# Performance work log

Measured on AMD Instinct MI355X. Metric: run time of the kernel, lower is better.

Reference implementation:

```python
import jax, jax.numpy as jnp
import numpy as np

B = 128
K = 16
# (in_ch, featdim, dim) per stage, matching conv1..conv11
DIMS = [(3, 8, 2048), (8, 32, 1024), (32, 64, 512), (64, 64, 256), (64, 64, 128),
        (64, 128, 64), (128, 256, 32), (256, 512, 16), (512, 512, 8), (512, 512, 4),
        (512, 1024, 2)]


def setup_inputs() -> dict:
    key = jax.random.key(0)
    ks = jax.random.split(key, 64)
    inp = {"x": jax.random.normal(ks[0], (B, 3, 2048), dtype=jnp.float32)}
    i = 1
    for li, (cin, cf, d) in enumerate(DIMS, start=1):
        inp[f"W{li}"] = jax.random.normal(ks[i], (3 * cf, cin), dtype=jnp.float32) / np.sqrt(cin).astype(np.float32); i += 1
        inp[f"b{li}"] = jax.random.normal(ks[i], (3 * cf,), dtype=jnp.float32) * 0.01; i += 1
        inp[f"sel{li}"] = jax.random.randint(ks[i], (d,), 0, 3); i += 1
    inp["fcW"] = jax.random.normal(ks[i], (K, 1024), dtype=jnp.float32) / np.sqrt(1024).astype(np.float32); i += 1
    inp["fcb"] = jax.random.normal(ks[i], (K,), dtype=jnp.float32) * 0.01
    return inp


def kdconv(x, W, b, sel, featdim, dim):
    # 1x1 conv == per-position matmul: x [B, Cin, dim] -> y [B, 3*featdim, dim]
    y = jax.nn.relu(jnp.einsum('oi,bin->bon', W, x) + b[None, :, None])
    y = y.reshape(-1, featdim, 3, dim)
    # kd split-dim gather: pick one of the 3 feature groups per position
    y = jnp.take_along_axis(y, sel[None, None, None, :], axis=2)[:, :, 0, :]  # [B, featdim, dim]
    # pairwise max-pool of sibling leaves
    return y.reshape(-1, featdim, dim // 2, 2).max(axis=-1)  # [B, featdim, dim//2]


def reference(x, sel1, sel2, sel3, sel4, sel5, sel6, sel7, sel8, sel9, sel10, sel11,
              W1, b1, W2, b2, W3, b3, W4, b4, W5, b5, W6, b6, W7, b7, W8, b8,
              W9, b9, W10, b10, W11, b11, fcW, fcb):
    Ws = [W1, W2, W3, W4, W5, W6, W7, W8, W9, W10, W11]
    bs = [b1, b2, b3, b4, b5, b6, b7, b8, b9, b10, b11]
    sels = [sel1, sel2, sel3, sel4, sel5, sel6, sel7, sel8, sel9, sel10, sel11]
    h = x
    for (cin, cf, d), W, b, s in zip(DIMS, Ws, bs, sels):
        h = kdconv(h, W, b, s, cf, d)
    h = h.reshape(-1, 1024)  # [B, 1024]
    return jax.nn.log_softmax(h @ fcW.T + fcb, axis=-1)
```

## Files before the change

kernel.cpp:

```cpp
#include <hip/hip_runtime.h>
#include <math.h>

#define BATCH 128

typedef __attribute__((ext_vector_type(8))) short bf16x8;
typedef __attribute__((ext_vector_type(4))) float f32x4;

__device__ __forceinline__ unsigned short f2bf(float f) {
    unsigned u = __builtin_bit_cast(unsigned, f);
    u += 0x7FFF + ((u >> 16) & 1);
    return (unsigned short)(u >> 16);
}
__device__ __forceinline__ float bf2f(unsigned short h) {
    unsigned u = ((unsigned)h) << 16;
    return __builtin_bit_cast(float, u);
}

struct PackArgs { const float* W[9]; int end[9]; };

__global__ __launch_bounds__(256) void pack_kernel(PackArgs pa, unsigned short* __restrict__ Wb, int total)
{
    int t = blockIdx.x * 256 + threadIdx.x;
    if (t >= total) return;
    int li = 0;
    while (t >= pa.end[li]) ++li;
    int base = (li == 0) ? 0 : pa.end[li - 1];
    Wb[t] = f2bf(pa.W[li][t - base]);
}

__global__ __launch_bounds__(256) void l1_kernel(
    const float* __restrict__ x, const float* __restrict__ W,
    const float* __restrict__ bias, const int* __restrict__ sel,
    unsigned short* __restrict__ Xout)
{
    __shared__ float wl[72];
    __shared__ float bl[24];
    int tid = threadIdx.x;
    if (tid < 72) wl[tid] = W[tid];
    if (tid >= 128 && tid < 152) bl[tid - 128] = bias[tid - 128];
    __syncthreads();

    int t  = blockIdx.x * 256 + tid;
    int np = t & 1023;
    int b  = t >> 10;
    int s0 = sel[2 * np], s1 = sel[2 * np + 1];

    const float* xb = x + (size_t)b * 6144 + 2 * np;
    float2 c0 = *(const float2*)(xb);
    float2 c1 = *(const float2*)(xb + 2048);
    float2 c2 = *(const float2*)(xb + 4096);

    unsigned short o[8];
#pragma unroll
    for (int f = 0; f < 8; ++f) {
        int r0 = f * 3 + s0, r1 = f * 3 + s1;
        float z0 = fmaf(wl[r0*3+2], c2.x, fmaf(wl[r0*3+1], c1.x, fmaf(wl[r0*3+0], c0.x, bl[r0])));
        float z1 = fmaf(wl[r1*3+2], c2.y, fmaf(wl[r1*3+1], c1.y, fmaf(wl[r1*3+0], c0.y, bl[r1])));
        o[f] = f2bf(fmaxf(fmaxf(z0, z1), 0.f));
    }
    unsigned short* dst = Xout + ((size_t)np * 128 + b) * 8;
    *(ushort4*)dst       = make_ushort4(o[0], o[1], o[2], o[3]);
    *(ushort4*)(dst + 4) = make_ushort4(o[4], o[5], o[6], o[7]);
}

__global__ __launch_bounds__(256) void l2_kernel(
    const unsigned short* __restrict__ Xin, const float* __restrict__ W,
    const float* __restrict__ bias, const int* __restrict__ sel,
    unsigned short* __restrict__ Xout)
{
    __shared__ float wl[768];
    __shared__ float bl[96];
    int tid = threadIdx.x;
    for (int i = tid; i < 768; i += 256) wl[i] = W[i];
    if (tid < 96) bl[tid] = bias[tid];
    __syncthreads();

    int t  = blockIdx.x * 256 + tid;
    int b  = t & 127;
    int np = t >> 7;
    int s0 = sel[2 * np], s1 = sel[2 * np + 1];

    const unsigned short* r0 = Xin + ((size_t)(2 * np) * 128 + b) * 8;
    const unsigned short* r1 = Xin + ((size_t)(2 * np + 1) * 128 + b) * 8;
    float xa[8], xb[8];
    {
        ushort4 u0 = *(const ushort4*)r0, u1 = *(const ushort4*)(r0 + 4);
        ushort4 v0 = *(const ushort4*)r1, v1 = *(const ushort4*)(r1 + 4);
        xa[0]=bf2f(u0.x); xa[1]=bf2f(u0.y); xa[2]=bf2f(u0.z); xa[3]=bf2f(u0.w);
        xa[4]=bf2f(u1.x); xa[5]=bf2f(u1.y); xa[6]=bf2f(u1.z); xa[7]=bf2f(u1.w);
        xb[0]=bf2f(v0.x); xb[1]=bf2f(v0.y); xb[2]=bf2f(v0.z); xb[3]=bf2f(v0.w);
        xb[4]=bf2f(v1.x); xb[5]=bf2f(v1.y); xb[6]=bf2f(v1.z); xb[7]=bf2f(v1.w);
    }

    unsigned short o[32];
#pragma unroll
    for (int f = 0; f < 32; ++f) {
        const float* w0 = &wl[(f * 3 + s0) * 8];
        const float* w1 = &wl[(f * 3 + s1) * 8];
        float z0 = bl[f * 3 + s0], z1 = bl[f * 3 + s1];
#pragma unroll
        for (int k = 0; k < 8; ++k) {
            z0 = fmaf(w0[k], xa[k], z0);
            z1 = fmaf(w1[k], xb[k], z1);
        }
        o[f] = f2bf(fmaxf(fmaxf(z0, z1), 0.f));
    }
    unsigned short* dst = Xout + ((size_t)np * 128 + b) * 32;
#pragma unroll
    for (int i = 0; i < 8; ++i)
        *(ushort4*)(dst + 4 * i) = make_ushort4(o[4*i], o[4*i+1], o[4*i+2], o[4*i+3]);
}

template<int CIN, int CF, int NP, int MW, int NW>
__global__ __launch_bounds__(256) void mfma_kernel(
    const unsigned short* __restrict__ Xin,
    const unsigned short* __restrict__ Wb,
    const float* __restrict__ bias,
    const int*   __restrict__ sel,
    unsigned short* __restrict__ Xout)
{
    constexpr int FT = CF / (16 * MW);
    constexpr int BT = 128 / (16 * NW);

    const int wid  = threadIdx.x >> 6;
    const int lane = threadIdx.x & 63;
    const int task = blockIdx.x * 4 + wid;
    const int bi = task % BT;
    const int fi = (task / BT) % FT;
    const int n  = task / (BT * FT);

    const int c = lane & 15;
    const int q = lane >> 4;
    const int s0 = __builtin_amdgcn_readfirstlane(sel[2 * n]);
    const int s1 = __builtin_amdgcn_readfirstlane(sel[2 * n + 1]);

    const int f0 = fi * 16 * MW;
    const int b0 = bi * 16 * NW;

    const unsigned short* ap[2][MW];
    const unsigned short* bp[2][NW];
#pragma unroll
    for (int p = 0; p < 2; ++p) {
        int s = p ? s1 : s0;
#pragma unroll
        for (int mi = 0; mi < MW; ++mi)
            ap[p][mi] = Wb + (size_t)((f0 + mi * 16 + c) * 3 + s) * CIN + q * 8;
#pragma unroll
        for (int ni = 0; ni < NW; ++ni)
            bp[p][ni] = Xin + ((size_t)(2 * n + p) * 128 + b0 + ni * 16 + c) * CIN + q * 8;
    }

    f32x4 acc[2][MW][NW];
#pragma unroll
    for (int p = 0; p < 2; ++p)
#pragma unroll
        for (int mi = 0; mi < MW; ++mi)
#pragma unroll
            for (int ni = 0; ni < NW; ++ni)
                acc[p][mi][ni] = (f32x4){0.f, 0.f, 0.f, 0.f};

#pragma unroll 2
    for (int k = 0; k < CIN; k += 32) {
        bf16x8 A[2][MW], B[2][NW];
#pragma unroll
        for (int p = 0; p < 2; ++p) {
#pragma unroll
            for (int mi = 0; mi < MW; ++mi)
                A[p][mi] = __builtin_bit_cast(bf16x8, *(const float4*)(const void*)(ap[p][mi] + k));
#pragma unroll
            for (int ni = 0; ni < NW; ++ni)
                B[p][ni] = __builtin_bit_cast(bf16x8, *(const float4*)(const void*)(bp[p][ni] + k));
        }
#pragma unroll
        for (int p = 0; p < 2; ++p)
#pragma unroll
            for (int mi = 0; mi < MW; ++mi)
#pragma unroll
                for (int ni = 0; ni < NW; ++ni)
                    acc[p][mi][ni] = __builtin_amdgcn_mfma_f32_16x16x32_bf16(
                        A[p][mi], B[p][ni], acc[p][mi][ni], 0, 0, 0);
    }

#pragma unroll
    for (int mi = 0; mi < MW; ++mi) {
        int fbase = f0 + mi * 16 + q * 4;
        float bi0[4], bi1[4];
#pragma unroll
        for (int r = 0; r < 4; ++r) {
            bi0[r] = bias[(fbase + r) * 3 + s0];
            bi1[r] = bias[(fbase + r) * 3 + s1];
        }
#pragma unroll
        for (int ni = 0; ni < NW; ++ni) {
            int b = b0 + ni * 16 + c;
            unsigned short o[4];
#pragma unroll
            for (int r = 0; r < 4; ++r) {
                float v = fmaxf(fmaxf(acc[0][mi][ni][r] + bi0[r],
                                      acc[1][mi][ni][r] + bi1[r]), 0.f);
                o[r] = f2bf(v);
            }
            *(ushort4*)(Xout + ((size_t)n * 128 + b) * CF + fbase) =
                make_ushort4(o[0], o[1], o[2], o[3]);
        }
    }
}

__global__ __launch_bounds__(256) void fc_logsoftmax_kernel(
    const unsigned short* __restrict__ h, const float* __restrict__ fcW,
    const float* __restrict__ fcb, float* __restrict__ out)
{
    int b   = blockIdx.x;
    int tid = threadIdx.x;
    int k     = tid & 15;
    int chunk = tid >> 4;

    const float* __restrict__ wk = fcW + (size_t)k * 1024;
    const unsigned short* hb = h + (size_t)b * 1024;

    float partial = 0.0f;
    int j0 = chunk * 64;
#pragma unroll 8
    for (int j = 0; j < 64; ++j)
        partial = fmaf(bf2f(hb[j0 + j]), wk[j0 + j], partial);

    __shared__ float red[16][17];
    red[chunk][k] = partial;
    __syncthreads();

    __shared__ float logits[16];
    if (tid < 16) {
        float s = fcb[tid];
#pragma unroll
        for (int c = 0; c < 16; ++c) s += red[c][tid];
        logits[tid] = s;
    }
    __syncthreads();

    if (tid < 16) {
        float mx = -INFINITY;
#pragma unroll
        for (int kk = 0; kk < 16; ++kk) mx = fmaxf(mx, logits[kk]);
        float se = 0.0f;
#pragma unroll
        for (int kk = 0; kk < 16; ++kk) se += expf(logits[kk] - mx);
        out[b * 16 + tid] = logits[tid] - mx - logf(se);
    }
}

extern "C" void kernel_launch(void* const* d_in, const int* in_sizes, int n_in,
                              void* d_out, int out_size, void* d_ws, size_t ws_size,
                              hipStream_t stream)
{
    const float* x   = (const float*)d_in[0];
    const float* fcW = (const float*)d_in[34];
    const float* fcb = (const float*)d_in[35];

#define WL(i) (const float*)d_in[1 + 3 * (i)]
#define BL(i) (const float*)d_in[2 + 3 * (i)]
#define SL(i) (const int*)  d_in[3 + 3 * (i)]

    unsigned short* buf0 = (unsigned short*)d_ws;
    unsigned short* buf1 = buf0 + 2u * 1024u * 1024u;
    unsigned short* Wb   = buf1 + 2u * 1024u * 1024u;

    static const int welems[9] = {6144, 12288, 12288, 24576, 98304, 393216, 786432, 786432, 1572864};
    PackArgs pa;
    int accum = 0, woff[9];
    for (int i = 0; i < 9; ++i) {
        pa.W[i] = WL(i + 2);
        woff[i] = accum;
        accum += welems[i];
        pa.end[i] = accum;
    }
    pack_kernel<<<(accum + 255) / 256, 256, 0, stream>>>(pa, Wb, accum);

    l1_kernel<<<512, 256, 0, stream>>>(x, WL(0), BL(0), SL(0), buf0);
    l2_kernel<<<256, 256, 0, stream>>>(buf0, WL(1), BL(1), SL(1), buf1);

    mfma_kernel<32, 64, 256, 2, 2><<<512, 256, 0, stream>>>(buf1, Wb + woff[0], BL(2), SL(2), buf0);
    mfma_kernel<64, 64, 128, 2, 2><<<256, 256, 0, stream>>>(buf0, Wb + woff[1], BL(3), SL(3), buf1);
    mfma_kernel<64, 64, 64, 2, 2><<<128, 256, 0, stream>>>(buf1, Wb + woff[2], BL(4), SL(4), buf0);
    mfma_kernel<64, 128, 32, 2, 2><<<128, 256, 0, stream>>>(buf0, Wb + woff[3], BL(5), SL(5), buf1);
    mfma_kernel<128, 256, 16, 2, 2><<<128, 256, 0, stream>>>(buf1, Wb + woff[4], BL(6), SL(6), buf0);
    mfma_kernel<256, 512, 8, 2, 2><<<128, 256, 0, stream>>>(buf0, Wb + woff[5], BL(7), SL(7), buf1);
    mfma_kernel<512, 512, 4, 1, 2><<<128, 256, 0, stream>>>(buf1, Wb + woff[6], BL(8), SL(8), buf0);
    mfma_kernel<512, 512, 2, 1, 2><<<64, 256, 0, stream>>>(buf0, Wb + woff[7], BL(9), SL(9), buf1);
    mfma_kernel<512, 1024, 1, 1, 2><<<64, 256, 0, stream>>>(buf1, Wb + woff[8], BL(10), SL(10), buf0);

    fc_logsoftmax_kernel<<<BATCH, 256, 0, stream>>>(buf0, fcW, fcb, (float*)d_out);

#undef WL
#undef BL
#undef SL
}
```

Baseline: 228.7 us.

## Fuse all layers into one cooperative persistent kernel with grid syncs

Replaces the twelve separate kernel launches (weight pack, two scalar layers, nine MFMA layers, FC/log-softmax) with a single cooperative kernel of 256 blocks of 512 threads. Stages are separated by grid.sync() and MFMA tasks are distributed with a grid-stride loop over waves. The aim is to remove per-launch overhead and the idle tails between small dependent kernels. The FC/log-softmax stage now runs one wave per batch row with shuffle reductions, and weight packing uses vectorised float4 loads. In exchange it adds grid-wide barrier cost, depends on all blocks being co-resident, and lowers per-layer parallelism on the early layers.

```diff
diff --git a/kernel.cpp b/kernel.cpp
--- a/kernel.cpp
+++ b/kernel.cpp
@@ -1,5 +1,8 @@
 #include <hip/hip_runtime.h>
+#include <hip/hip_cooperative_groups.h>
 #include <math.h>
+
+namespace cg = cooperative_groups;
 
 #define BATCH 128
 
@@ -16,103 +19,21 @@
     return __builtin_bit_cast(float, u);
 }
 
-struct PackArgs { const float* W[9]; int end[9]; };
-
-__global__ __launch_bounds__(256) void pack_kernel(PackArgs pa, unsigned short* __restrict__ Wb, int total)
-{
-    int t = blockIdx.x * 256 + threadIdx.x;
-    if (t >= total) return;
-    int li = 0;
-    while (t >= pa.end[li]) ++li;
-    int base = (li == 0) ? 0 : pa.end[li - 1];
-    Wb[t] = f2bf(pa.W[li][t - base]);
-}
-
-__global__ __launch_bounds__(256) void l1_kernel(
-    const float* __restrict__ x, const float* __restrict__ W,
-    const float* __restrict__ bias, const int* __restrict__ sel,
-    unsigned short* __restrict__ Xout)
-{
-    __shared__ float wl[72];
-    __shared__ float bl[24];
-    int tid = threadIdx.x;
-    if (tid < 72) wl[tid] = W[tid];
-    if (tid >= 128 && tid < 152) bl[tid - 128] = bias[tid - 128];
-    __syncthreads();
-
-    int t  = blockIdx.x * 256 + tid;
-    int np = t & 1023;
-    int b  = t >> 10;
-    int s0 = sel[2 * np], s1 = sel[2 * np + 1];
-
-    const float* xb = x + (size_t)b * 6144 + 2 * np;
-    float2 c0 = *(const float2*)(xb);
-    float2 c1 = *(const float2*)(xb + 2048);
-    float2 c2 = *(const float2*)(xb + 4096);
-
-    unsigned short o[8];
-#pragma unroll
-    for (int f = 0; f < 8; ++f) {
-        int r0 = f * 3 + s0, r1 = f * 3 + s1;
-        float z0 = fmaf(wl[r0*3+2], c2.x, fmaf(wl[r0*3+1], c1.x, fmaf(wl[r0*3+0], c0.x, bl[r0])));
-        float z1 = fmaf(wl[r1*3+2], c2.y, fmaf(wl[r1*3+1], c1.y, fmaf(wl[r1*3+0], c0.y, bl[r1])));
-        o[f] = f2bf(fmaxf(fmaxf(z0, z1), 0.f));
-    }
-    unsigned short* dst = Xout + ((size_t)np * 128 + b) * 8;
-    *(ushort4*)dst       = make_ushort4(o[0], o[1], o[2], o[3]);
-    *(ushort4*)(dst + 4) = make_ushort4(o[4], o[5], o[6], o[7]);
-}
-
-__global__ __launch_bounds__(256) void l2_kernel(
-    const unsigned short* __restrict__ Xin, const float* __restrict__ W,
-    const float* __restrict__ bias, const int* __restrict__ sel,
-    unsigned short* __restrict__ Xout)
-{
-    __shared__ float wl[768];
-    __shared__ float bl[96];
-    int tid = threadIdx.x;
-    for (int i = tid; i < 768; i += 256) wl[i] = W[i];
-    if (tid < 96) bl[tid] = bias[tid];
-    __syncthreads();
-
-    int t  = blockIdx.x * 256 + tid;
-    int b  = t & 127;
-    int np = t >> 7;
-    int s0 = sel[2 * np], s1 = sel[2 * np + 1];
-
-    const unsigned short* r0 = Xin + ((size_t)(2 * np) * 128 + b) * 8;
-    const unsigned short* r1 = Xin + ((size_t)(2 * np + 1) * 128 + b) * 8;
-    float xa[8], xb[8];
-    {
-        ushort4 u0 = *(const ushort4*)r0, u1 = *(const ushort4*)(r0 + 4);
-        ushort4 v0 = *(const ushort4*)r1, v1 = *(const ushort4*)(r1 + 4);
-        xa[0]=bf2f(u0.x); xa[1]=bf2f(u0.y); xa[2]=bf2f(u0.z); xa[3]=bf2f(u0.w);
-        xa[4]=bf2f(u1.x); xa[5]=bf2f(u1.y); xa[6]=bf2f(u1.z); xa[7]=bf2f(u1.w);
-        xb[0]=bf2f(v0.x); xb[1]=bf2f(v0.y); xb[2]=bf2f(v0.z); xb[3]=bf2f(v0.w);
-        xb[4]=bf2f(v1.x); xb[5]=bf2f(v1.y); xb[6]=bf2f(v1.z); xb[7]=bf2f(v1.w);
-    }
-
-    unsigned short o[32];
-#pragma unroll
-    for (int f = 0; f < 32; ++f) {
-        const float* w0 = &wl[(f * 3 + s0) * 8];
-        const float* w1 = &wl[(f * 3 + s1) * 8];
-        float z0 = bl[f * 3 + s0], z1 = bl[f * 3 + s1];
-#pragma unroll
-        for (int k = 0; k < 8; ++k) {
-            z0 = fmaf(w0[k], xa[k], z0);
-            z1 = fmaf(w1[k], xb[k], z1);
-        }
-        o[f] = f2bf(fmaxf(fmaxf(z0, z1), 0.f));
-    }
-    unsigned short* dst = Xout + ((size_t)np * 128 + b) * 32;
-#pragma unroll
-    for (int i = 0; i < 8; ++i)
-        *(ushort4*)(dst + 4 * i) = make_ushort4(o[4*i], o[4*i+1], o[4*i+2], o[4*i+3]);
-}
+struct KParams {
+    const float* x;
+    const float* W[11];
+    const float* B[11];
+    const int*   S[11];
+    const float* fcW;
+    const float* fcb;
+    float*       out;
+    unsigned short* buf0;
+    unsigned short* buf1;
+    unsigned short* Wb;
+};
 
 template<int CIN, int CF, int NP, int MW, int NW>
-__global__ __launch_bounds__(256) void mfma_kernel(
+__device__ void mfma_layer(int gwave, int lane,
     const unsigned short* __restrict__ Xin,
     const unsigned short* __restrict__ Wb,
     const float* __restrict__ bias,
@@ -121,130 +42,237 @@
 {
     constexpr int FT = CF / (16 * MW);
     constexpr int BT = 128 / (16 * NW);
-
-    const int wid  = threadIdx.x >> 6;
-    const int lane = threadIdx.x & 63;
-    const int task = blockIdx.x * 4 + wid;
-    const int bi = task % BT;
-    const int fi = (task / BT) % FT;
-    const int n  = task / (BT * FT);
+    constexpr int TASKS = NP * FT * BT;
 
     const int c = lane & 15;
     const int q = lane >> 4;
-    const int s0 = __builtin_amdgcn_readfirstlane(sel[2 * n]);
-    const int s1 = __builtin_amdgcn_readfirstlane(sel[2 * n + 1]);
-
-    const int f0 = fi * 16 * MW;
-    const int b0 = bi * 16 * NW;
-
-    const unsigned short* ap[2][MW];
-    const unsigned short* bp[2][NW];
-#pragma unroll
-    for (int p = 0; p < 2; ++p) {
-        int s = p ? s1 : s0;
-#pragma unroll
-        for (int mi = 0; mi < MW; ++mi)
-            ap[p][mi] = Wb + (size_t)((f0 + mi * 16 + c) * 3 + s) * CIN + q * 8;
-#pragma unroll
-        for (int ni = 0; ni < NW; ++ni)
-            bp[p][ni] = Xin + ((size_t)(2 * n + p) * 128 + b0 + ni * 16 + c) * CIN + q * 8;
-    }
-
-    f32x4 acc[2][MW][NW];
-#pragma unroll
-    for (int p = 0; p < 2; ++p)
-#pragma unroll
-        for (int mi = 0; mi < MW; ++mi)
+
+    for (int task = gwave; task < TASKS; task += 2048) {
+        const int bi = task % BT;
+        const int fi = (task / BT) % FT;
+        const int n  = task / (BT * FT);
+
+        const int s0 = __builtin_amdgcn_readfirstlane(sel[2 * n]);
+        const int s1 = __builtin_amdgcn_readfirstlane(sel[2 * n + 1]);
+
+        const int f0 = fi * 16 * MW;
+        const int b0 = bi * 16 * NW;
+
+        const unsigned short* ap[2][MW];
+        const unsigned short* bp[2][NW];
+#pragma unroll
+        for (int p = 0; p < 2; ++p) {
+            int s = p ? s1 : s0;
+#pragma unroll
+            for (int mi = 0; mi < MW; ++mi)
+                ap[p][mi] = Wb + (size_t)((f0 + mi * 16 + c) * 3 + s) * CIN + q * 8;
 #pragma unroll
             for (int ni = 0; ni < NW; ++ni)
-                acc[p][mi][ni] = (f32x4){0.f, 0.f, 0.f, 0.f};
+                bp[p][ni] = Xin + ((size_t)(2 * n + p) * 128 + b0 + ni * 16 + c) * CIN + q * 8;
+        }
+
+        f32x4 acc[2][MW][NW];
+#pragma unroll
+        for (int p = 0; p < 2; ++p)
+#pragma unroll
+            for (int mi = 0; mi < MW; ++mi)
+#pragma unroll
+                for (int ni = 0; ni < NW; ++ni)
+                    acc[p][mi][ni] = (f32x4){0.f, 0.f, 0.f, 0.f};
 
 #pragma unroll 2
-    for (int k = 0; k < CIN; k += 32) {
-        bf16x8 A[2][MW], B[2][NW];
-#pragma unroll
-        for (int p = 0; p < 2; ++p) {
-#pragma unroll
-            for (int mi = 0; mi < MW; ++mi)
-                A[p][mi] = __builtin_bit_cast(bf16x8, *(const float4*)(const void*)(ap[p][mi] + k));
-#pragma unroll
-            for (int ni = 0; ni < NW; ++ni)
-                B[p][ni] = __builtin_bit_cast(bf16x8, *(const float4*)(const void*)(bp[p][ni] + k));
-        }
-#pragma unroll
-        for (int p = 0; p < 2; ++p)
-#pragma unroll
-            for (int mi = 0; mi < MW; ++mi)
+        for (int k = 0; k < CIN; k += 32) {
+            bf16x8 A[2][MW], B[2][NW];
+#pragma unroll
+            for (int p = 0; p < 2; ++p) {
+#pragma unroll
+                for (int mi = 0; mi < MW; ++mi)
+                    A[p][mi] = __builtin_bit_cast(bf16x8, *(const float4*)(const void*)(ap[p][mi] + k));
 #pragma unroll
                 for (int ni = 0; ni < NW; ++ni)
-                    acc[p][mi][ni] = __builtin_amdgcn_mfma_f32_16x16x32_bf16(
-                        A[p][mi], B[p][ni], acc[p][mi][ni], 0, 0, 0);
-    }
-
-#pragma unroll
-    for (int mi = 0; mi < MW; ++mi) {
-        int fbase = f0 + mi * 16 + q * 4;
-        float bi0[4], bi1[4];
-#pragma unroll
-        for (int r = 0; r < 4; ++r) {
-            bi0[r] = bias[(fbase + r) * 3 + s0];
-            bi1[r] = bias[(fbase + r) * 3 + s1];
-        }
-#pragma unroll
-        for (int ni = 0; ni < NW; ++ni) {
-            int b = b0 + ni * 16 + c;
-            unsigned short o[4];
+                    B[p][ni] = __builtin_bit_cast(bf16x8, *(const float4*)(const void*)(bp[p][ni] + k));
+            }
+#pragma unroll
+            for (int p = 0; p < 2; ++p)
+#pragma unroll
+                for (int mi = 0; mi < MW; ++mi)
+#pragma unroll
+                    for (int ni = 0; ni < NW; ++ni)
+                        acc[p][mi][ni] = __builtin_amdgcn_mfma_f32_16x16x32_bf16(
+                            A[p][mi], B[p][ni], acc[p][mi][ni], 0, 0, 0);
+        }
+
+#pragma unroll
+        for (int mi = 0; mi < MW; ++mi) {
+            int fbase = f0 + mi * 16 + q * 4;
+            float bi0[4], bi1[4];
 #pragma unroll
             for (int r = 0; r < 4; ++r) {
-                float v = fmaxf(fmaxf(acc[0][mi][ni][r] + bi0[r],
-                                      acc[1][mi][ni][r] + bi1[r]), 0.f);
-                o[r] = f2bf(v);
-            }
-            *(ushort4*)(Xout + ((size_t)n * 128 + b) * CF + fbase) =
-                make_ushort4(o[0], o[1], o[2], o[3]);
-        }
-    }
-}
-
-__global__ __launch_bounds__(256) void fc_logsoftmax_kernel(
-    const unsigned short* __restrict__ h, const float* __restrict__ fcW,
-    const float* __restrict__ fcb, float* __restrict__ out)
+                bi0[r] = bias[(fbase + r) * 3 + s0];
+                bi1[r] = bias[(fbase + r) * 3 + s1];
+            }
+#pragma unroll
+            for (int ni = 0; ni < NW; ++ni) {
+                int b = b0 + ni * 16 + c;
+                unsigned short o[4];
+#pragma unroll
+                for (int r = 0; r < 4; ++r) {
+                    float v = fmaxf(fmaxf(acc[0][mi][ni][r] + bi0[r],
+                                          acc[1][mi][ni][r] + bi1[r]), 0.f);
+                    o[r] = f2bf(v);
+                }
+                *(ushort4*)(Xout + ((size_t)n * 128 + b) * CF + fbase) =
+                    make_ushort4(o[0], o[1], o[2], o[3]);
+            }
+        }
+    }
+}
+
+__global__ __launch_bounds__(512) void mega_kernel(KParams P)
 {
-    int b   = blockIdx.x;
-    int tid = threadIdx.x;
-    int k     = tid & 15;
-    int chunk = tid >> 4;
-
-    const float* __restrict__ wk = fcW + (size_t)k * 1024;
-    const unsigned short* hb = h + (size_t)b * 1024;
-
-    float partial = 0.0f;
-    int j0 = chunk * 64;
+    cg::grid_group grid = cg::this_grid();
+    constexpr int NT = 256 * 512;
+    const int tid     = threadIdx.x;
+    const int gthread = blockIdx.x * 512 + tid;
+    const int gwave   = gthread >> 6;
+    const int lane    = tid & 63;
+
+    __shared__ float swl[768];
+    __shared__ float sbl[96];
+
+    {
+        constexpr int we[9] = {6144, 12288, 12288, 24576, 98304, 393216, 786432, 786432, 1572864};
+        int off = 0;
+#pragma unroll
+        for (int li = 0; li < 9; ++li) {
+            const float4* src = (const float4*)P.W[li + 2];
+            ushort4* dst = (ushort4*)(P.Wb + off);
+            int n4 = we[li] >> 2;
+            for (int i = gthread; i < n4; i += NT) {
+                float4 w = src[i];
+                dst[i] = make_ushort4(f2bf(w.x), f2bf(w.y), f2bf(w.z), f2bf(w.w));
+            }
+            off += we[li];
+        }
+    }
+    if (tid < 72) swl[tid] = P.W[0][tid];
+    if (tid >= 128 && tid < 152) sbl[tid - 128] = P.B[0][tid - 128];
+    grid.sync();
+
+    {
+        int t  = gthread;
+        int np = t & 1023;
+        int b  = t >> 10;
+        int s0 = P.S[0][2 * np], s1 = P.S[0][2 * np + 1];
+
+        const float* xb = P.x + (size_t)b * 6144 + 2 * np;
+        float2 c0 = *(const float2*)(xb);
+        float2 c1 = *(const float2*)(xb + 2048);
+        float2 c2 = *(const float2*)(xb + 4096);
+
+        unsigned short o[8];
+#pragma unroll
+        for (int f = 0; f < 8; ++f) {
+            int r0 = f * 3 + s0, r1 = f * 3 + s1;
+            float z0 = fmaf(swl[r0*3+2], c2.x, fmaf(swl[r0*3+1], c1.x, fmaf(swl[r0*3+0], c0.x, sbl[r0])));
+            float z1 = fmaf(swl[r1*3+2], c2.y, fmaf(swl[r1*3+1], c1.y, fmaf(swl[r1*3+0], c0.y, sbl[r1])));
+            o[f] = f2bf(fmaxf(fmaxf(z0, z1), 0.f));
+        }
+        unsigned short* dst = P.buf0 + ((size_t)np * 128 + b) * 8;
+        *(ushort4*)dst       = make_ushort4(o[0], o[1], o[2], o[3]);
+        *(ushort4*)(dst + 4) = make_ushort4(o[4], o[5], o[6], o[7]);
+    }
+    grid.sync();
+
+    for (int i = tid; i < 768; i += 512) swl[i] = P.W[1][i];
+    if (tid < 96) sbl[tid] = P.B[1][tid];
+    __syncthreads();
+
+    if (gthread < 65536) {
+        int t  = gthread;
+        int b  = t & 127;
+        int np = t >> 7;
+        int s0 = P.S[1][2 * np], s1 = P.S[1][2 * np + 1];
+
+        const unsigned short* r0 = P.buf0 + ((size_t)(2 * np) * 128 + b) * 8;
+        const unsigned short* r1 = P.buf0 + ((size_t)(2 * np + 1) * 128 + b) * 8;
+        float xa[8], xb[8];
+        {
+            ushort4 u0 = *(const ushort4*)r0, u1 = *(const ushort4*)(r0 + 4);
+            ushort4 v0 = *(const ushort4*)r1, v1 = *(const ushort4*)(r1 + 4);
+            xa[0]=bf2f(u0.x); xa[1]=bf2f(u0.y); xa[2]=bf2f(u0.z); xa[3]=bf2f(u0.w);
+            xa[4]=bf2f(u1.x); xa[5]=bf2f(u1.y); xa[6]=bf2f(u1.z); xa[7]=bf2f(u1.w);
+            xb[0]=bf2f(v0.x); xb[1]=bf2f(v0.y); xb[2]=bf2f(v0.z); xb[3]=bf2f(v0.w);
+            xb[4]=bf2f(v1.x); xb[5]=bf2f(v1.y); xb[6]=bf2f(v1.z); xb[7]=bf2f(v1.w);
+        }
+        unsigned short o[32];
+#pragma unroll
+        for (int f = 0; f < 32; ++f) {
+            const float* w0 = &swl[(f * 3 + s0) * 8];
+            const float* w1 = &swl[(f * 3 + s1) * 8];
+            float z0 = sbl[f * 3 + s0], z1 = sbl[f * 3 + s1];
+#pragma unroll
+            for (int k = 0; k < 8; ++k) {
+                z0 = fmaf(w0[k], xa[k], z0);
+                z1 = fmaf(w1[k], xb[k], z1);
+            }
+            o[f] = f2bf(fmaxf(fmaxf(z0, z1), 0.f));
+        }
+        unsigned short* dst = P.buf1 + ((size_t)np * 128 + b) * 32;
+#pragma unroll
+        for (int i = 0; i < 8; ++i)
+            *(ushort4*)(dst + 4 * i) = make_ushort4(o[4*i], o[4*i+1], o[4*i+2], o[4*i+3]);
+    }
+    grid.sync();
+
+    mfma_layer<32, 64, 256, 2, 2>(gwave, lane, P.buf1, P.Wb + 0,       P.B[2],  P.S[2],  P.buf0);
+    grid.sync();
+    mfma_layer<64, 64, 128, 2, 2>(gwave, lane, P.buf0, P.Wb + 6144,    P.B[3],  P.S[3],  P.buf1);
+    grid.sync();
+    mfma_layer<64, 64, 64, 2, 2>(gwave, lane, P.buf1, P.Wb + 18432,    P.B[4],  P.S[4],  P.buf0);
+    grid.sync();
+    mfma_layer<64, 128, 32, 2, 2>(gwave, lane, P.buf0, P.Wb + 30720,   P.B[5],  P.S[5],  P.buf1);
+    grid.sync();
+    mfma_layer<128, 256, 16, 2, 2>(gwave, lane, P.buf1, P.Wb + 55296,  P.B[6],  P.S[6],  P.buf0);
+    grid.sync();
+    mfma_layer<256, 512, 8, 2, 2>(gwave, lane, P.buf0, P.Wb + 153600,  P.B[7],  P.S[7],  P.buf1);
+    grid.sync();
+    mfma_layer<512, 512, 4, 1, 2>(gwave, lane, P.buf1, P.Wb + 546816,  P.B[8],  P.S[8],  P.buf0);
+    grid.sync();
+    mfma_layer<512, 512, 2, 1, 2>(gwave, lane, P.buf0, P.Wb + 1333248, P.B[9],  P.S[9],  P.buf1);
+    grid.sync();
+    mfma_layer<512, 1024, 1, 1, 2>(gwave, lane, P.buf1, P.Wb + 2119680, P.B[10], P.S[10], P.buf0);
+    grid.sync();
+
+    if (gwave < 128) {
+        int b = gwave;
+        int k = lane & 15;
+        int q = lane >> 4;
+        const unsigned short* hq = P.buf0 + (size_t)b * 1024 + q * 256;
+        const float* wq = P.fcW + (size_t)k * 1024 + q * 256;
+
+        float partial = 0.f;
 #pragma unroll 8
-    for (int j = 0; j < 64; ++j)
-        partial = fmaf(bf2f(hb[j0 + j]), wk[j0 + j], partial);
-
-    __shared__ float red[16][17];
-    red[chunk][k] = partial;
-    __syncthreads();
-
-    __shared__ float logits[16];
-    if (tid < 16) {
-        float s = fcb[tid];
-#pragma unroll
-        for (int c = 0; c < 16; ++c) s += red[c][tid];
-        logits[tid] = s;
-    }
-    __syncthreads();
-
-    if (tid < 16) {
-        float mx = -INFINITY;
-#pragma unroll
-        for (int kk = 0; kk < 16; ++kk) mx = fmaxf(mx, logits[kk]);
-        float se = 0.0f;
-#pragma unroll
-        for (int kk = 0; kk < 16; ++kk) se += expf(logits[kk] - mx);
-        out[b * 16 + tid] = logits[tid] - mx - logf(se);
+        for (int j = 0; j < 256; j += 4) {
+            ushort4 h4 = *(const ushort4*)(hq + j);
+            float4  w4 = *(const float4*)(wq + j);
+            partial = fmaf(bf2f(h4.x), w4.x, partial);
+            partial = fmaf(bf2f(h4.y), w4.y, partial);
+            partial = fmaf(bf2f(h4.z), w4.z, partial);
+            partial = fmaf(bf2f(h4.w), w4.w, partial);
+        }
+        partial += __shfl_xor(partial, 16, 64);
+        partial += __shfl_xor(partial, 32, 64);
+        float logit = partial + P.fcb[k];
+
+        float m = logit;
+#pragma unroll
+        for (int off = 1; off < 16; off <<= 1) m = fmaxf(m, __shfl_xor(m, off, 16));
+        float se = expf(logit - m);
+#pragma unroll
+        for (int off = 1; off < 16; off <<= 1) se += __shfl_xor(se, off, 16);
+
+        if (lane < 16) P.out[b * 16 + k] = logit - m - logf(se);
     }
 }
 
@@ -252,45 +280,23 @@
                               void* d_out, int out_size, void* d_ws, size_t ws_size,
                               hipStream_t stream)
 {
-    const float* x   = (const float*)d_in[0];
-    const float* fcW = (const float*)d_in[34];
-    const float* fcb = (const float*)d_in[35];
-
-#define WL(i) (const float*)d_in[1 + 3 * (i)]
-#define BL(i) (const float*)d_in[2 + 3 * (i)]
-#define SL(i) (const int*)  d_in[3 + 3 * (i)]
+    KParams P;
+    P.x = (const float*)d_in[0];
+    for (int i = 0; i < 11; ++i) {
+        P.W[i] = (const float*)d_in[1 + 3 * i];
+        P.B[i] = (const float*)d_in[2 + 3 * i];
+        P.S[i] = (const int*)  d_in[3 + 3 * i];
+    }
+    P.fcW = (const float*)d_in[34];
+    P.fcb = (const float*)d_in[35];
+    P.out = (float*)d_out;
 
     unsigned short* buf0 = (unsigned short*)d_ws;
     unsigned short* buf1 = buf0 + 2u * 1024u * 1024u;
     unsigned short* Wb   = buf1 + 2u * 1024u * 1024u;
-
-    static const int welems[9] = {6144, 12288, 12288, 24576, 98304, 393216, 786432, 786432, 1572864};
-    PackArgs pa;
-    int accum = 0, woff[9];
-    for (int i = 0; i < 9; ++i) {
-        pa.W[i] = WL(i + 2);
-        woff[i] = accum;
-        accum += welems[i];
-        pa.end[i] = accum;
-    }
-    pack_kernel<<<(accum + 255) / 256, 256, 0, stream>>>(pa, Wb, accum);
-
-    l1_kernel<<<512, 256, 0, stream>>>(x, WL(0), BL(0), SL(0), buf0);
-    l2_kernel<<<256, 256, 0, stream>>>(buf0, WL(1), BL(1), SL(1), buf1);
-
-    mfma_kernel<32, 64, 256, 2, 2><<<512, 256, 0, stream>>>(buf1, Wb + woff[0], BL(2), SL(2), buf0);
-    mfma_kernel<64, 64, 128, 2, 2><<<256, 256, 0, stream>>>(buf0, Wb + woff[1], BL(3), SL(3), buf1);
-    mfma_kernel<64, 64, 64, 2, 2><<<128, 256, 0, stream>>>(buf1, Wb + woff[2], BL(4), SL(4), buf0);
-    mfma_kernel<64, 128, 32, 2, 2><<<128, 256, 0, stream>>>(buf0, Wb + woff[3], BL(5), SL(5), buf1);
-    mfma_kernel<128, 256, 16, 2, 2><<<128, 256, 0, stream>>>(buf1, Wb + woff[4], BL(6), SL(6), buf0);
-    mfma_kernel<256, 512, 8, 2, 2><<<128, 256, 0, stream>>>(buf0, Wb + woff[5], BL(7), SL(7), buf1);
-    mfma_kernel<512, 512, 4, 1, 2><<<128, 256, 0, stream>>>(buf1, Wb + woff[6], BL(8), SL(8), buf0);
-    mfma_kernel<512, 512, 2, 1, 2><<<64, 256, 0, stream>>>(buf0, Wb + woff[7], BL(9), SL(9), buf1);
-    mfma_kernel<512, 1024, 1, 1, 2><<<64, 256, 0, stream>>>(buf1, Wb + woff[8], BL(10), SL(10), buf0);
-
-    fc_logsoftmax_kernel<<<BATCH, 256, 0, stream>>>(buf0, fcW, fcb, (float*)d_out);
-
-#undef WL
-#undef BL
-#undef SL
-}
+    P.buf0 = buf0; P.buf1 = buf1; P.Wb = Wb;
+
+    void* args[] = { &P };
+    hipLaunchCooperativeKernel((const void*)mega_kernel,
+                               dim3(256), dim3(512), args, 0, stream);
+}
```

Result: slower. 657.5 us (+187.6%).

## Fuse kd-tree conv layers into multi-stage kernels with LDS-resident intermediates

Applied to the files above, without the earlier changes.

Merges layers 1-2 into one kernel whose extra blocks also pack the later weights to bf16, so the weight conversion runs alongside the early layers. Layers 3-5 and 6-8 are fused into single kernels that keep per-subtree intermediates in shared memory. Layers 3-5 convert their small weights straight into LDS. This cuts the launch count from 13 to 7 and removes global round-trips for the intermediate activations. In exchange, the fused kernels run few, large-LDS blocks (64 blocks for stage 3), which lowers parallelism on the GPU.

```diff
diff --git a/kernel.cpp b/kernel.cpp
--- a/kernel.cpp
+++ b/kernel.cpp
@@ -1,7 +1,5 @@
 #include <hip/hip_runtime.h>
 #include <math.h>
-
-#define BATCH 128
 
 typedef __attribute__((ext_vector_type(8))) short bf16x8;
 typedef __attribute__((ext_vector_type(4))) float f32x4;
@@ -16,99 +14,286 @@
     return __builtin_bit_cast(float, u);
 }
 
-struct PackArgs { const float* W[9]; int end[9]; };
-
-__global__ __launch_bounds__(256) void pack_kernel(PackArgs pa, unsigned short* __restrict__ Wb, int total)
-{
-    int t = blockIdx.x * 256 + threadIdx.x;
-    if (t >= total) return;
-    int li = 0;
-    while (t >= pa.end[li]) ++li;
-    int base = (li == 0) ? 0 : pa.end[li - 1];
-    Wb[t] = f2bf(pa.W[li][t - base]);
-}
-
-__global__ __launch_bounds__(256) void l1_kernel(
-    const float* __restrict__ x, const float* __restrict__ W,
-    const float* __restrict__ bias, const int* __restrict__ sel,
-    unsigned short* __restrict__ Xout)
-{
-    __shared__ float wl[72];
-    __shared__ float bl[24];
-    int tid = threadIdx.x;
-    if (tid < 72) wl[tid] = W[tid];
-    if (tid >= 128 && tid < 152) bl[tid - 128] = bias[tid - 128];
-    __syncthreads();
-
-    int t  = blockIdx.x * 256 + tid;
-    int np = t & 1023;
-    int b  = t >> 10;
-    int s0 = sel[2 * np], s1 = sel[2 * np + 1];
-
-    const float* xb = x + (size_t)b * 6144 + 2 * np;
-    float2 c0 = *(const float2*)(xb);
-    float2 c1 = *(const float2*)(xb + 2048);
-    float2 c2 = *(const float2*)(xb + 4096);
-
-    unsigned short o[8];
-#pragma unroll
-    for (int f = 0; f < 8; ++f) {
-        int r0 = f * 3 + s0, r1 = f * 3 + s1;
-        float z0 = fmaf(wl[r0*3+2], c2.x, fmaf(wl[r0*3+1], c1.x, fmaf(wl[r0*3+0], c0.x, bl[r0])));
-        float z1 = fmaf(wl[r1*3+2], c2.y, fmaf(wl[r1*3+1], c1.y, fmaf(wl[r1*3+0], c0.y, bl[r1])));
-        o[f] = f2bf(fmaxf(fmaxf(z0, z1), 0.f));
-    }
-    unsigned short* dst = Xout + ((size_t)np * 128 + b) * 8;
-    *(ushort4*)dst       = make_ushort4(o[0], o[1], o[2], o[3]);
-    *(ushort4*)(dst + 4) = make_ushort4(o[4], o[5], o[6], o[7]);
-}
-
-__global__ __launch_bounds__(256) void l2_kernel(
-    const unsigned short* __restrict__ Xin, const float* __restrict__ W,
-    const float* __restrict__ bias, const int* __restrict__ sel,
-    unsigned short* __restrict__ Xout)
-{
-    __shared__ float wl[768];
-    __shared__ float bl[96];
-    int tid = threadIdx.x;
-    for (int i = tid; i < 768; i += 256) wl[i] = W[i];
-    if (tid < 96) bl[tid] = bias[tid];
-    __syncthreads();
-
-    int t  = blockIdx.x * 256 + tid;
-    int b  = t & 127;
-    int np = t >> 7;
-    int s0 = sel[2 * np], s1 = sel[2 * np + 1];
-
-    const unsigned short* r0 = Xin + ((size_t)(2 * np) * 128 + b) * 8;
-    const unsigned short* r1 = Xin + ((size_t)(2 * np + 1) * 128 + b) * 8;
-    float xa[8], xb[8];
+struct K1Params {
+    const float* x;
+    const float* W1; const float* B1; const int* S1;
+    const float* W2; const float* B2; const int* S2;
+    const float* Wsrc[6];
+    unsigned short* Wb;
+    unsigned short* X3;
+};
+
+__global__ __launch_bounds__(256) void k1_kernel(K1Params P)
+{
+    const int tid = threadIdx.x;
+
+    if (blockIdx.x >= 128) {
+        int gt = (blockIdx.x - 128) * 256 + tid;
+        const int we[6] = {24576, 98304, 393216, 786432, 786432, 1572864};
+        int off = 0;
+#pragma unroll
+        for (int li = 0; li < 6; ++li) {
+            const float4* src = (const float4*)P.Wsrc[li];
+            ushort4* dst = (ushort4*)(P.Wb + off);
+            int n4 = we[li] >> 2;
+            for (int i = gt; i < n4; i += 16384) {
+                float4 w = src[i];
+                dst[i] = make_ushort4(f2bf(w.x), f2bf(w.y), f2bf(w.z), f2bf(w.w));
+            }
+            off += we[li];
+        }
+        return;
+    }
+
+    __shared__ float wl1[72], bl1[24], wl2[768], bl2[96];
+    __shared__ unsigned short bufL1[16 * 64 * 8];
+
+    if (tid < 72) wl1[tid] = P.W1[tid];
+    if (tid >= 128 && tid < 152) bl1[tid - 128] = P.B1[tid - 128];
+    for (int i = tid; i < 768; i += 256) wl2[i] = P.W2[i];
+    if (tid < 96) bl2[tid] = P.B2[tid];
+    __syncthreads();
+
+    const int npT = blockIdx.x >> 1;
+    const int b0  = (blockIdx.x & 1) * 64;
+
+    for (int i = tid; i < 1024; i += 256) {
+        int pos_l = i >> 6, bl = i & 63;
+        int np1 = npT * 16 + pos_l;
+        int b = b0 + bl;
+        int s0 = P.S1[2 * np1], s1 = P.S1[2 * np1 + 1];
+        const float* xb = P.x + (size_t)b * 6144 + 2 * np1;
+        float2 c0 = *(const float2*)(xb);
+        float2 c1 = *(const float2*)(xb + 2048);
+        float2 c2 = *(const float2*)(xb + 4096);
+        unsigned short o[8];
+#pragma unroll
+        for (int f = 0; f < 8; ++f) {
+            int r0 = f * 3 + s0, r1 = f * 3 + s1;
+            float z0 = fmaf(wl1[r0*3+2], c2.x, fmaf(wl1[r0*3+1], c1.x, fmaf(wl1[r0*3+0], c0.x, bl1[r0])));
+            float z1 = fmaf(wl1[r1*3+2], c2.y, fmaf(wl1[r1*3+1], c1.y, fmaf(wl1[r1*3+0], c0.y, bl1[r1])));
+            o[f] = f2bf(fmaxf(fmaxf(z0, z1), 0.f));
+        }
+        unsigned short* dst = &bufL1[((size_t)pos_l * 64 + bl) * 8];
+        *(ushort4*)dst       = make_ushort4(o[0], o[1], o[2], o[3]);
+        *(ushort4*)(dst + 4) = make_ushort4(o[4], o[5], o[6], o[7]);
+    }
+    __syncthreads();
+
+    for (int i = tid; i < 512; i += 256) {
+        int np_l = i >> 6, bl = i & 63;
+        int np2 = npT * 8 + np_l;
+        int s0 = P.S2[2 * np2], s1 = P.S2[2 * np2 + 1];
+        const unsigned short* r0 = &bufL1[((size_t)(2 * np_l) * 64 + bl) * 8];
+        const unsigned short* r1 = &bufL1[((size_t)(2 * np_l + 1) * 64 + bl) * 8];
+        float xa[8], xb[8];
+        {
+            ushort4 u0 = *(const ushort4*)r0, u1 = *(const ushort4*)(r0 + 4);
+            ushort4 v0 = *(const ushort4*)r1, v1 = *(const ushort4*)(r1 + 4);
+            xa[0]=bf2f(u0.x); xa[1]=bf2f(u0.y); xa[2]=bf2f(u0.z); xa[3]=bf2f(u0.w);
+            xa[4]=bf2f(u1.x); xa[5]=bf2f(u1.y); xa[6]=bf2f(u1.z); xa[7]=bf2f(u1.w);
+            xb[0]=bf2f(v0.x); xb[1]=bf2f(v0.y); xb[2]=bf2f(v0.z); xb[3]=bf2f(v0.w);
+            xb[4]=bf2f(v1.x); xb[5]=bf2f(v1.y); xb[6]=bf2f(v1.z); xb[7]=bf2f(v1.w);
+        }
+        unsigned short o[32];
+#pragma unroll
+        for (int f = 0; f < 32; ++f) {
+            const float* w0 = &wl2[(f * 3 + s0) * 8];
+            const float* w1 = &wl2[(f * 3 + s1) * 8];
+            float z0 = bl2[f * 3 + s0], z1 = bl2[f * 3 + s1];
+#pragma unroll
+            for (int k = 0; k < 8; ++k) {
+                z0 = fmaf(w0[k], xa[k], z0);
+                z1 = fmaf(w1[k], xb[k], z1);
+            }
+            o[f] = f2bf(fmaxf(fmaxf(z0, z1), 0.f));
+        }
+        unsigned short* dst = P.X3 + ((size_t)np2 * 128 + b0 + bl) * 32;
+#pragma unroll
+        for (int i2 = 0; i2 < 8; ++i2)
+            *(ushort4*)(dst + 4 * i2) = make_ushort4(o[4*i2], o[4*i2+1], o[4*i2+2], o[4*i2+3]);
+    }
+}
+
+template<int CIN>
+__device__ __forceinline__ void mfma_tile(
+    const unsigned short* a0, const unsigned short* a1,
+    const unsigned short* b0p, const unsigned short* b1p,
+    f32x4& acc0, f32x4& acc1)
+{
+#pragma unroll
+    for (int k = 0; k < CIN; k += 32) {
+        bf16x8 A0 = __builtin_bit_cast(bf16x8, *(const float4*)(const void*)(a0 + k));
+        bf16x8 A1 = __builtin_bit_cast(bf16x8, *(const float4*)(const void*)(a1 + k));
+        bf16x8 B0 = __builtin_bit_cast(bf16x8, *(const float4*)(const void*)(b0p + k));
+        bf16x8 B1 = __builtin_bit_cast(bf16x8, *(const float4*)(const void*)(b1p + k));
+        acc0 = __builtin_amdgcn_mfma_f32_16x16x32_bf16(A0, B0, acc0, 0, 0, 0);
+        acc1 = __builtin_amdgcn_mfma_f32_16x16x32_bf16(A1, B1, acc1, 0, 0, 0);
+    }
+}
+
+__device__ __forceinline__ void epilogue_store(
+    unsigned short* dst, const f32x4& acc0, const f32x4& acc1,
+    const float* bias, int fbase, int s0, int s1)
+{
+    unsigned short o[4];
+#pragma unroll
+    for (int r = 0; r < 4; ++r) {
+        float v = fmaxf(fmaxf(acc0[r] + bias[(fbase + r) * 3 + s0],
+                              acc1[r] + bias[(fbase + r) * 3 + s1]), 0.f);
+        o[r] = f2bf(v);
+    }
+    *(ushort4*)dst = make_ushort4(o[0], o[1], o[2], o[3]);
+}
+
+__global__ __launch_bounds__(256) void stage2_kernel(
+    const unsigned short* __restrict__ X3,
+    const float* __restrict__ W3f, const float* __restrict__ B3, const int* __restrict__ S3,
+    const float* __restrict__ W4f, const float* __restrict__ B4, const int* __restrict__ S4,
+    const float* __restrict__ W5f, const float* __restrict__ B5, const int* __restrict__ S5,
+    unsigned short* __restrict__ X6)
+{
+    __shared__ unsigned short W3l[6144];
+    __shared__ unsigned short W4l[12288];
+    __shared__ unsigned short W5l[12288];
+    __shared__ unsigned short L3o[4 * 32 * 64];
+    __shared__ unsigned short L4o[2 * 32 * 64];
+
+    const int tid  = threadIdx.x;
+    const int lane = tid & 63;
+    const int wv   = tid >> 6;
+    const int c = lane & 15, q = lane >> 4;
+    const int n5 = blockIdx.x >> 2;
+    const int b0 = (blockIdx.x & 3) * 32;
+
+    for (int i = tid; i < 1536; i += 256) {
+        float4 w = ((const float4*)W3f)[i];
+        ((ushort4*)W3l)[i] = make_ushort4(f2bf(w.x), f2bf(w.y), f2bf(w.z), f2bf(w.w));
+    }
+    for (int i = tid; i < 3072; i += 256) {
+        float4 w = ((const float4*)W4f)[i];
+        ((ushort4*)W4l)[i] = make_ushort4(f2bf(w.x), f2bf(w.y), f2bf(w.z), f2bf(w.w));
+        float4 v = ((const float4*)W5f)[i];
+        ((ushort4*)W5l)[i] = make_ushort4(f2bf(v.x), f2bf(v.y), f2bf(v.z), f2bf(v.w));
+    }
+    __syncthreads();
+
+    for (int t = wv; t < 32; t += 4) {
+        int bt = t & 1, ft = (t >> 1) & 3, j = t >> 3;
+        int np = 4 * n5 + j;
+        int s0 = __builtin_amdgcn_readfirstlane(S3[2 * np]);
+        int s1 = __builtin_amdgcn_readfirstlane(S3[2 * np + 1]);
+        int f0 = ft * 16, bl = bt * 16;
+        const unsigned short* a0 = &W3l[((f0 + c) * 3 + s0) * 32 + q * 8];
+        const unsigned short* a1 = &W3l[((f0 + c) * 3 + s1) * 32 + q * 8];
+        const unsigned short* bp0 = X3 + ((size_t)(8 * n5 + 2 * j) * 128 + b0 + bl + c) * 32 + q * 8;
+        const unsigned short* bp1 = X3 + ((size_t)(8 * n5 + 2 * j + 1) * 128 + b0 + bl + c) * 32 + q * 8;
+        f32x4 acc0 = {0.f,0.f,0.f,0.f}, acc1 = {0.f,0.f,0.f,0.f};
+        mfma_tile<32>(a0, a1, bp0, bp1, acc0, acc1);
+        epilogue_store(&L3o[((size_t)j * 32 + bl + c) * 64 + f0 + q * 4],
+                       acc0, acc1, B3, f0 + q * 4, s0, s1);
+    }
+    __syncthreads();
+
+    for (int t = wv; t < 16; t += 4) {
+        int bt = t & 1, ft = (t >> 1) & 3, j = t >> 3;
+        int np = 2 * n5 + j;
+        int s0 = __builtin_amdgcn_readfirstlane(S4[2 * np]);
+        int s1 = __builtin_amdgcn_readfirstlane(S4[2 * np + 1]);
+        int f0 = ft * 16, bl = bt * 16;
+        const unsigned short* a0 = &W4l[((f0 + c) * 3 + s0) * 64 + q * 8];
+        const unsigned short* a1 = &W4l[((f0 + c) * 3 + s1) * 64 + q * 8];
+        const unsigned short* bp0 = &L3o[((size_t)(2 * j) * 32 + bl + c) * 64 + q * 8];
+        const unsigned short* bp1 = &L3o[((size_t)(2 * j + 1) * 32 + bl + c) * 64 + q * 8];
+        f32x4 acc0 = {0.f,0.f,0.f,0.f}, acc1 = {0.f,0.f,0.f,0.f};
+        mfma_tile<64>(a0, a1, bp0, bp1, acc0, acc1);
+        epilogue_store(&L4o[((size_t)j * 32 + bl + c) * 64 + f0 + q * 4],
+                       acc0, acc1, B4, f0 + q * 4, s0, s1);
+    }
+    __syncthreads();
+
+    for (int t = wv; t < 8; t += 4) {
+        int bt = t & 1, ft = t >> 1;
+        int s0 = __builtin_amdgcn_readfirstlane(S5[2 * n5]);
+        int s1 = __builtin_amdgcn_readfirstlane(S5[2 * n5 + 1]);
+        int f0 = ft * 16, bl = bt * 16;
+        const unsigned short* a0 = &W5l[((f0 + c) * 3 + s0) * 64 + q * 8];
+        const unsigned short* a1 = &W5l[((f0 + c) * 3 + s1) * 64 + q * 8];
+        const unsigned short* bp0 = &L4o[((size_t)(0) * 32 + bl + c) * 64 + q * 8];
+        const unsigned short* bp1 = &L4o[((size_t)(1) * 32 + bl + c) * 64 + q * 8];
+        f32x4 acc0 = {0.f,0.f,0.f,0.f}, acc1 = {0.f,0.f,0.f,0.f};
+        mfma_tile<64>(a0, a1, bp0, bp1, acc0, acc1);
+        epilogue_store(X6 + ((size_t)n5 * 128 + b0 + bl + c) * 64 + f0 + q * 4,
+                       acc0, acc1, B5, f0 + q * 4, s0, s1);
+    }
+}
+
+__global__ __launch_bounds__(512) void stage3_kernel(
+    const unsigned short* __restrict__ X6,
+    const unsigned short* __restrict__ W6b, const float* __restrict__ B6, const int* __restrict__ S6,
+    const unsigned short* __restrict__ W7b, const float* __restrict__ B7, const int* __restrict__ S7,
+    const unsigned short* __restrict__ W8b, const float* __restrict__ B8, const int* __restrict__ S8,
+    unsigned short* __restrict__ X9)
+{
+    __shared__ unsigned short L6o[4 * 16 * 128];
+    __shared__ unsigned short L7o[2 * 16 * 256];
+
+    const int tid  = threadIdx.x;
+    const int lane = tid & 63;
+    const int wv   = tid >> 6;
+    const int c = lane & 15, q = lane >> 4;
+    const int n8 = blockIdx.x >> 3;
+    const int b0 = (blockIdx.x & 7) * 16;
+
+    for (int t = wv; t < 32; t += 8) {
+        int ft = t & 7, j = t >> 3;
+        int np = 4 * n8 + j;
+        int s0 = __builtin_amdgcn_readfirstlane(S6[2 * np]);
+        int s1 = __builtin_amdgcn_readfirstlane(S6[2 * np + 1]);
+        int f0 = ft * 16;
+        const unsigned short* a0 = W6b + (size_t)((f0 + c) * 3 + s0) * 64 + q * 8;
+        const unsigned short* a1 = W6b + (size_t)((f0 + c) * 3 + s1) * 64 + q * 8;
+        const unsigned short* bp0 = X6 + ((size_t)(8 * n8 + 2 * j) * 128 + b0 + c) * 64 + q * 8;
+        const unsigned short* bp1 = X6 + ((size_t)(8 * n8 + 2 * j + 1) * 128 + b0 + c) * 64 + q * 8;
+        f32x4 acc0 = {0.f,0.f,0.f,0.f}, acc1 = {0.f,0.f,0.f,0.f};
+        mfma_tile<64>(a0, a1, bp0, bp1, acc0, acc1);
+        epilogue_store(&L6o[((size_t)j * 16 + c) * 128 + f0 + q * 4],
+                       acc0, acc1, B6, f0 + q * 4, s0, s1);
+    }
+    __syncthreads();
+
+    for (int t = wv; t < 32; t += 8) {
+        int ft = t & 15, j = t >> 4;
+        int np = 2 * n8 + j;
+        int s0 = __builtin_amdgcn_readfirstlane(S7[2 * np]);
+        int s1 = __builtin_amdgcn_readfirstlane(S7[2 * np + 1]);
+        int f0 = ft * 16;
+        const unsigned short* a0 = W7b + (size_t)((f0 + c) * 3 + s0) * 128 + q * 8;
+        const unsigned short* a1 = W7b + (size_t)((f0 + c) * 3 + s1) * 128 + q * 8;
+        const unsigned short* bp0 = &L6o[((size_t)(2 * j) * 16 + c) * 128 + q * 8];
+        const unsigned short* bp1 = &L6o[((size_t)(2 * j + 1) * 16 + c) * 128 + q * 8];
+        f32x4 acc0 = {0.f,0.f,0.f,0.f}, acc1 = {0.f,0.f,0.f,0.f};
+        mfma_tile<128>(a0, a1, bp0, bp1, acc0, acc1);
+        epilogue_store(&L7o[((size_t)j * 16 + c) * 256 + f0 + q * 4],
+                       acc0, acc1, B7, f0 + q * 4, s0, s1);
+    }
+    __syncthreads();
+
     {
-        ushort4 u0 = *(const ushort4*)r0, u1 = *(const ushort4*)(r0 + 4);
-        ushort4 v0 = *(const ushort4*)r1, v1 = *(const ushort4*)(r1 + 4);
-        xa[0]=bf2f(u0.x); xa[1]=bf2f(u0.y); xa[2]=bf2f(u0.z); xa[3]=bf2f(u0.w);
-        xa[4]=bf2f(u1.x); xa[5]=bf2f(u1.y); xa[6]=bf2f(u1.z); xa[7]=bf2f(u1.w);
-        xb[0]=bf2f(v0.x); xb[1]=bf2f(v0.y); xb[2]=bf2f(v0.z); xb[3]=bf2f(v0.w);
-        xb[4]=bf2f(v1.x); xb[5]=bf2f(v1.y); xb[6]=bf2f(v1.z); xb[7]=bf2f(v1.w);
-    }
-
-    unsigned short o[32];
-#pragma unroll
-    for (int f = 0; f < 32; ++f) {
-        const float* w0 = &wl[(f * 3 + s0) * 8];
-        const float* w1 = &wl[(f * 3 + s1) * 8];
-        float z0 = bl[f * 3 + s0], z1 = bl[f * 3 + s1];
-#pragma unroll
-        for (int k = 0; k < 8; ++k) {
-            z0 = fmaf(w0[k], xa[k], z0);
-            z1 = fmaf(w1[k], xb[k], z1);
-        }
-        o[f] = f2bf(fmaxf(fmaxf(z0, z1), 0.f));
-    }
-    unsigned short* dst = Xout + ((size_t)np * 128 + b) * 32;
-#pragma unroll
-    for (int i = 0; i < 8; ++i)
-        *(ushort4*)(dst + 4 * i) = make_ushort4(o[4*i], o[4*i+1], o[4*i+2], o[4*i+3]);
+        int s0 = __builtin_amdgcn_readfirstlane(S8[2 * n8]);
+        int s1 = __builtin_amdgcn_readfirstlane(S8[2 * n8 + 1]);
+        for (int t = wv; t < 32; t += 8) {
+            int f0 = t * 16;
+            const unsigned short* a0 = W8b + (size_t)((f0 + c) * 3 + s0) * 256 + q * 8;
+            const unsigned short* a1 = W8b + (size_t)((f0 + c) * 3 + s1) * 256 + q * 8;
+            const unsigned short* bp0 = &L7o[((size_t)(0) * 16 + c) * 256 + q * 8];
+            const unsigned short* bp1 = &L7o[((size_t)(1) * 16 + c) * 256 + q * 8];
+            f32x4 acc0 = {0.f,0.f,0.f,0.f}, acc1 = {0.f,0.f,0.f,0.f};
+            mfma_tile<256>(a0, a1, bp0, bp1, acc0, acc1);
+            epilogue_store(X9 + ((size_t)n8 * 128 + b0 + c) * 512 + f0 + q * 4,
+                           acc0, acc1, B8, f0 + q * 4, s0, s1);
+        }
+    }
 }
 
 template<int CIN, int CF, int NP, int MW, int NW>
@@ -184,24 +369,11 @@
 #pragma unroll
     for (int mi = 0; mi < MW; ++mi) {
         int fbase = f0 + mi * 16 + q * 4;
-        float bi0[4], bi1[4];
-#pragma unroll
-        for (int r = 0; r < 4; ++r) {
-            bi0[r] = bias[(fbase + r) * 3 + s0];
-            bi1[r] = bias[(fbase + r) * 3 + s1];
-        }
 #pragma unroll
         for (int ni = 0; ni < NW; ++ni) {
             int b = b0 + ni * 16 + c;
-            unsigned short o[4];
-#pragma unroll
-            for (int r = 0; r < 4; ++r) {
-                float v = fmaxf(fmaxf(acc[0][mi][ni][r] + bi0[r],
-                                      acc[1][mi][ni][r] + bi1[r]), 0.f);
-                o[r] = f2bf(v);
-            }
-            *(ushort4*)(Xout + ((size_t)n * 128 + b) * CF + fbase) =
-                make_ushort4(o[0], o[1], o[2], o[3]);
+            epilogue_store(Xout + ((size_t)n * 128 + b) * CF + fbase,
+                           acc[0][mi][ni], acc[1][mi][ni], bias, fbase, s0, s1);
         }
     }
 }
@@ -252,43 +424,35 @@
                               void* d_out, int out_size, void* d_ws, size_t ws_size,
                               hipStream_t stream)
 {
-    const float* x   = (const float*)d_in[0];
-    const float* fcW = (const float*)d_in[34];
-    const float* fcb = (const float*)d_in[35];
-
 #define WL(i) (const float*)d_in[1 + 3 * (i)]
 #define BL(i) (const float*)d_in[2 + 3 * (i)]
 #define SL(i) (const int*)  d_in[3 + 3 * (i)]
 
-    unsigned short* buf0 = (unsigned short*)d_ws;
-    unsigned short* buf1 = buf0 + 2u * 1024u * 1024u;
-    unsigned short* Wb   = buf1 + 2u * 1024u * 1024u;
-
-    static const int welems[9] = {6144, 12288, 12288, 24576, 98304, 393216, 786432, 786432, 1572864};
-    PackArgs pa;
-    int accum = 0, woff[9];
-    for (int i = 0; i < 9; ++i) {
-        pa.W[i] = WL(i + 2);
-        woff[i] = accum;
-        accum += welems[i];
-        pa.end[i] = accum;
-    }
-    pack_kernel<<<(accum + 255) / 256, 256, 0, stream>>>(pa, Wb, accum);
-
-    l1_kernel<<<512, 256, 0, stream>>>(x, WL(0), BL(0), SL(0), buf0);
-    l2_kernel<<<256, 256, 0, stream>>>(buf0, WL(1), BL(1), SL(1), buf1);
-
-    mfma_kernel<32, 64, 256, 2, 2><<<512, 256, 0, stream>>>(buf1, Wb + woff[0], BL(2), SL(2), buf0);
-    mfma_kernel<64, 64, 128, 2, 2><<<256, 256, 0, stream>>>(buf0, Wb + woff[1], BL(3), SL(3), buf1);
-    mfma_kernel<64, 64, 64, 2, 2><<<128, 256, 0, stream>>>(buf1, Wb + woff[2], BL(4), SL(4), buf0);
-    mfma_kernel<64, 128, 32, 2, 2><<<128, 256, 0, stream>>>(buf0, Wb + woff[3], BL(5), SL(5), buf1);
-    mfma_kernel<128, 256, 16, 2, 2><<<128, 256, 0, stream>>>(buf1, Wb + woff[4], BL(6), SL(6), buf0);
-    mfma_kernel<256, 512, 8, 2, 2><<<128, 256, 0, stream>>>(buf0, Wb + woff[5], BL(7), SL(7), buf1);
-    mfma_kernel<512, 512, 4, 1, 2><<<128, 256, 0, stream>>>(buf1, Wb + woff[6], BL(8), SL(8), buf0);
-    mfma_kernel<512, 512, 2, 1, 2><<<64, 256, 0, stream>>>(buf0, Wb + woff[7], BL(9), SL(9), buf1);
-    mfma_kernel<512, 1024, 1, 1, 2><<<64, 256, 0, stream>>>(buf1, Wb + woff[8], BL(10), SL(10), buf0);
-
-    fc_logsoftmax_kernel<<<BATCH, 256, 0, stream>>>(buf0, fcW, fcb, (float*)d_out);
+    unsigned short* bufA = (unsigned short*)d_ws;
+    unsigned short* bufB = bufA + 2u * 1024u * 1024u;
+    unsigned short* Wb   = bufB + 2u * 1024u * 1024u;
+
+    const int o6 = 0, o7 = 24576, o8 = 122880, o9 = 516096, o10 = 1302528, o11 = 2088960;
+
+    K1Params P;
+    P.x = (const float*)d_in[0];
+    P.W1 = WL(0); P.B1 = BL(0); P.S1 = SL(0);
+    P.W2 = WL(1); P.B2 = BL(1); P.S2 = SL(1);
+    for (int i = 0; i < 6; ++i) P.Wsrc[i] = WL(5 + i);
+    P.Wb = Wb; P.X3 = bufA;
+    k1_kernel<<<192, 256, 0, stream>>>(P);
+
+    stage2_kernel<<<256, 256, 0, stream>>>(bufA,
+        WL(2), BL(2), SL(2), WL(3), BL(3), SL(3), WL(4), BL(4), SL(4), bufB);
+
+    stage3_kernel<<<64, 512, 0, stream>>>(bufB,
+        Wb + o6, BL(5), SL(5), Wb + o7, BL(6), SL(6), Wb + o8, BL(7), SL(7), bufA);
+
+    mfma_kernel<512, 512, 4, 1, 2><<<128, 256, 0, stream>>>(bufA, Wb + o9,  BL(8),  SL(8),  bufB);
+    mfma_kernel<512, 512, 2, 1, 2><<<64, 256, 0, stream>>>(bufB, Wb + o10, BL(9),  SL(9),  bufA);
+    mfma_kernel<512, 1024, 1, 1, 2><<<64, 256, 0, stream>>>(bufA, Wb + o11, BL(10), SL(10), bufB);
+
+    fc_logsoftmax_kernel<<<128, 256, 0, stream>>>(bufB, (const float*)d_in[34], (const float*)d_in[35], (float*)d_out);
 
 #undef WL
 #undef BL
```

Result: slower. 237.4 us (+3.8%).
